# Kernel tuning notes

Measured on AMD Instinct MI355X. Metric: run time of the kernel, lower is better.

## Reference

```python
import jax, jax.numpy as jnp
import numpy as np

STRIDE = 16
A = 9
PRE_NMS_TOP_N = 6000
POST_NMS_TOP_N = 300
NMS_THRESH = 0.7
MIN_SIZE = 16
H, W = 128, 192


def _generate_anchors(base_size=16, ratios=(0.5, 1.0, 2.0), scales=(8, 16, 32)):
    base = np.array([0, 0, base_size - 1, base_size - 1], dtype=np.float64)
    w = base[2] - base[0] + 1
    h = base[3] - base[1] + 1
    x_ctr = base[0] + 0.5 * (w - 1)
    y_ctr = base[1] + 0.5 * (h - 1)
    size = w * h
    ratios = np.array(ratios)
    ws = np.round(np.sqrt(size / ratios))
    hs = np.round(ws * ratios)
    ratio_anchors = np.stack([x_ctr - 0.5 * (ws - 1), y_ctr - 0.5 * (hs - 1),
                              x_ctr + 0.5 * (ws - 1), y_ctr + 0.5 * (hs - 1)], axis=1)
    out = []
    scales = np.array(scales)
    for a in ratio_anchors:
        aw = a[2] - a[0] + 1
        ah = a[3] - a[1] + 1
        xc = a[0] + 0.5 * (aw - 1)
        yc = a[1] + 0.5 * (ah - 1)
        ws2 = aw * scales
        hs2 = ah * scales
        out.append(np.stack([xc - 0.5 * (ws2 - 1), yc - 0.5 * (hs2 - 1),
                             xc + 0.5 * (ws2 - 1), yc + 0.5 * (hs2 - 1)], axis=1))
    return np.concatenate(out, axis=0).astype(np.float32)  # [9,4]


def setup_inputs() -> dict:
    key = jax.random.key(0)
    k1, k2 = jax.random.split(key)
    scores = jax.random.uniform(k1, (1, 2 * A, H, W), dtype=jnp.float32)
    bbox_deltas = 0.1 * jax.random.normal(k2, (1, 4 * A, H, W), dtype=jnp.float32)
    im_info = jnp.array([[H * STRIDE, W * STRIDE, 1.0]], dtype=jnp.float32)
    return {"scores": scores, "bbox_deltas": bbox_deltas, "im_info": im_info}


def _proposal_forward(scores, bbox_deltas, im_info):
    anchors_base = jnp.asarray(_generate_anchors())  # [A,4]
    sc = scores[:, A:, :, :]                          # fg scores [1,A,H,W]
    h, w = sc.shape[-2], sc.shape[-1]
    shift_x = (jnp.arange(w) * STRIDE).astype(sc.dtype)
    shift_y = (jnp.arange(h) * STRIDE).astype(sc.dtype)
    sy, sx = jnp.meshgrid(shift_y, shift_x, indexing='ij')
    shifts = jnp.stack([sx.ravel(), sy.ravel(), sx.ravel(), sy.ravel()], axis=1)  # [K,4]
    anchors = (anchors_base[None, :, :] + shifts[:, None, :]).reshape(-1, 4)      # [K*A,4]

    deltas = bbox_deltas.transpose(0, 2, 3, 1).reshape(-1, 4)
    deltas = jnp.concatenate([deltas[:, :2], jnp.clip(deltas[:, 2:], -10.0, 10.0)], axis=1)
    sc = sc.transpose(0, 2, 3, 1).reshape(-1)  # [K*A]

    widths = anchors[:, 2] - anchors[:, 0] + 1.0
    heights = anchors[:, 3] - anchors[:, 1] + 1.0
    ctr_x = anchors[:, 0] + 0.5 * widths
    ctr_y = anchors[:, 1] + 0.5 * heights
    dx, dy, dw, dh = deltas[:, 0], deltas[:, 1], deltas[:, 2], deltas[:, 3]
    pcx = dx * widths + ctr_x
    pcy = dy * heights + ctr_y
    pw = jnp.exp(dw) * widths
    ph = jnp.exp(dh) * heights
    x1 = pcx - 0.5 * pw
    y1 = pcy - 0.5 * ph
    x2 = pcx + 0.5 * pw
    y2 = pcy + 0.5 * ph

    info = im_info[0]
    x1 = jnp.clip(x1, 0.0, info[1] - 1.0)
    x2 = jnp.clip(x2, 0.0, info[1] - 1.0)
    y1 = jnp.clip(y1, 0.0, info[0] - 1.0)
    y2 = jnp.clip(y2, 0.0, info[0] - 1.0)
    proposals = jnp.stack([x1, y1, x2, y2], axis=1)

    # filter_boxes: mask (instead of dropping) boxes smaller than min_size*scale
    min_sz = MIN_SIZE * info[2]
    valid = ((x2 - x1 + 1.0) >= min_sz) & ((y2 - y1 + 1.0) >= min_sz)
    masked = jnp.where(valid, sc, -jnp.inf)

    # sort desc + pre_nms_topN
    top_scores, top_idx = jax.lax.top_k(masked, PRE_NMS_TOP_N)
    boxes = proposals[top_idx]               # [PRE,4], score-descending
    tvalid = top_scores > -jnp.inf

    # pairwise IoU (torchvision convention)
    area = (boxes[:, 2] - boxes[:, 0]) * (boxes[:, 3] - boxes[:, 1])
    lt = jnp.maximum(boxes[:, None, :2], boxes[None, :, :2])
    rb = jnp.minimum(boxes[:, None, 2:], boxes[None, :, 2:])
    wh = jnp.clip(rb - lt, 0.0)
    inter = wh[..., 0] * wh[..., 1]
    iou = inter / (area[:, None] + area[None, :] - inter)  # [PRE,PRE]

    # greedy NMS over score-sorted boxes
    n = PRE_NMS_TOP_N
    def step(keep, x):
        iou_col, v, i = x
        suppressed = jnp.any(keep & (iou_col > NMS_THRESH))
        k = v & jnp.logical_not(suppressed)
        keep = keep.at[i].set(k)
        return keep, k
    keep, _ = jax.lax.scan(step, jnp.zeros((n,), dtype=bool),
                           (iou.T, tvalid, jnp.arange(n)))

    # kept boxes first (stable => score order preserved), take post_nms_topN
    order = jnp.argsort(jnp.logical_not(keep).astype(jnp.int32), stable=True)[:POST_NMS_TOP_N]
    kept = keep[order]
    out_boxes = jnp.where(kept[:, None], boxes[order], 0.0)
    output = jnp.concatenate(
        [jnp.zeros((POST_NMS_TOP_N, 1), out_boxes.dtype), out_boxes], axis=1)
    return output  # [POST,5]: (batch_idx=0, x1,y1,x2,y2); rows beyond kept count are zero


def reference(scores, bbox_deltas, im_info):
    return _proposal_forward(scores, bbox_deltas, im_info)
```

## Files before the change

kernel.cpp:

```cpp
#include <hip/hip_runtime.h>

#define N_ANCH 221184
#define HW     24576
#define Wd     192
#define AA     9
#define TOPN   6000
#define POSTN  300
#define CAND_CAP 8192
#define NWORDS 94
#define NCHUNK 47

typedef unsigned long long u64;
typedef __attribute__((ext_vector_type(2))) unsigned long long u64x2;

__device__ const float c_aw[9] = {184.f,368.f,736.f,128.f,256.f,512.f, 88.f,176.f,352.f};
__device__ const float c_ah[9] = { 96.f,192.f,384.f,128.f,256.f,512.f,176.f,352.f,704.f};

__device__ __forceinline__ float4 decode_box(int a, int cell,
                                             const float* __restrict__ deltas,
                                             float info0, float info1, float info2,
                                             bool* valid) {
    int h = cell / Wd;
    int w = cell - h * Wd;
    const float* db = deltas + (size_t)(4 * a) * HW + cell;
    float dx = db[0];
    float dy = db[HW];
    float dw = db[2 * HW];
    float dh = db[3 * HW];
    dw = fminf(fmaxf(dw, -10.f), 10.f);
    dh = fminf(fmaxf(dh, -10.f), 10.f);

    float ww = c_aw[a], hh = c_ah[a];
    float cx = 16.f * (float)w + 8.f;
    float cy = 16.f * (float)h + 8.f;

    float pcx = __fadd_rn(__fmul_rn(dx, ww), cx);
    float pcy = __fadd_rn(__fmul_rn(dy, hh), cy);
    float pw  = __fmul_rn(expf(dw), ww);
    float ph  = __fmul_rn(expf(dh), hh);
    float hpw = __fmul_rn(0.5f, pw);
    float hph = __fmul_rn(0.5f, ph);
    float x1 = __fsub_rn(pcx, hpw);
    float x2 = __fadd_rn(pcx, hpw);
    float y1 = __fsub_rn(pcy, hph);
    float y2 = __fadd_rn(pcy, hph);

    float xmax = __fsub_rn(info1, 1.f);
    float ymax = __fsub_rn(info0, 1.f);
    x1 = fminf(fmaxf(x1, 0.f), xmax);
    x2 = fminf(fmaxf(x2, 0.f), xmax);
    y1 = fminf(fmaxf(y1, 0.f), ymax);
    y2 = fminf(fmaxf(y2, 0.f), ymax);

    float msz = __fmul_rn(16.f, info2);
    *valid = (__fadd_rn(__fsub_rn(x2, x1), 1.f) >= msz) &&
             (__fadd_rn(__fsub_rn(y2, y1), 1.f) >= msz);
    return make_float4(x1, y1, x2, y2);
}

#define ZA_F4 4164
#define ZB_F4 48
__global__ __launch_bounds__(256) void init_kernel(float4* zA, float4* zB) {
    int t = blockIdx.x * 256 + threadIdx.x;
    float4 z = make_float4(0.f, 0.f, 0.f, 0.f);
    if (t < ZA_F4) zA[t] = z;
    else if (t < ZA_F4 + ZB_F4) zB[t - ZA_F4] = z;
}

__global__ __launch_bounds__(256) void decode_kernel(const float* __restrict__ scores,
                                                     const float* __restrict__ deltas,
                                                     const float* __restrict__ iminfo,
                                                     unsigned int* __restrict__ keys,
                                                     unsigned int* __restrict__ hist256) {
    __shared__ unsigned int lh[256];
    lh[threadIdx.x] = 0u;
    __syncthreads();
    int t = blockIdx.x * 256 + threadIdx.x;
    int a = t / HW;
    int cell = t - a * HW;
    float score = scores[(AA + a) * HW + cell];
    bool valid;
    (void)decode_box(a, cell, deltas, iminfo[0], iminfo[1], iminfo[2], &valid);
    unsigned int sb = __float_as_uint(score);
    unsigned int key = valid ? ((sb & 0x80000000u) ? ~sb : (sb | 0x80000000u))
                             : 0x007FFFFFu;
    keys[t] = key;
    atomicAdd(&lh[key >> 24], 1u);
    __syncthreads();
    if (lh[threadIdx.x]) atomicAdd(&hist256[threadIdx.x], lh[threadIdx.x]);
}

__global__ __launch_bounds__(1024) void midselect_kernel(const unsigned int* __restrict__ keys,
                                                         const unsigned int* __restrict__ hist256,
                                                         unsigned int* __restrict__ state) {
    __shared__ unsigned int sfx[256];
    __shared__ unsigned int h2w[16][256];
    __shared__ unsigned int sP, sRank;
    int t = threadIdx.x;
    int wv = t >> 6;
    for (int i = t; i < 16 * 256; i += 1024) ((unsigned int*)h2w)[i] = 0u;
    if (t < 256) sfx[t] = hist256[t];
    __syncthreads();
    for (int d = 1; d < 256; d <<= 1) {
        unsigned int v = 0u;
        if (t < 256 && t + d < 256) v = sfx[t + d];
        __syncthreads();
        if (t < 256) sfx[t] += v;
        __syncthreads();
    }
    if (t < 256) {
        unsigned int ge = sfx[t];
        unsigned int gt = (t < 255) ? sfx[t + 1] : 0u;
        if (ge >= TOPN && gt < TOPN) { sP = (unsigned int)t; sRank = TOPN - gt; }
    }
    __syncthreads();
    unsigned int P = sP, rank = sRank;
    const uint4* k4 = (const uint4*)keys;
    for (int i = t; i < N_ANCH / 4; i += 1024) {
        uint4 v = k4[i];
        if ((v.x >> 24) == P) atomicAdd(&h2w[wv][(v.x >> 16) & 0xFFu], 1u);
        if ((v.y >> 24) == P) atomicAdd(&h2w[wv][(v.y >> 16) & 0xFFu], 1u);
        if ((v.z >> 24) == P) atomicAdd(&h2w[wv][(v.z >> 16) & 0xFFu], 1u);
        if ((v.w >> 24) == P) atomicAdd(&h2w[wv][(v.w >> 16) & 0xFFu], 1u);
    }
    __syncthreads();
    if (t < 256) {
        unsigned int s = 0;
        #pragma unroll
        for (int wvi = 0; wvi < 16; ++wvi) s += h2w[wvi][t];
        sfx[t] = s;
    }
    __syncthreads();
    for (int d = 1; d < 256; d <<= 1) {
        unsigned int v = 0u;
        if (t < 256 && t + d < 256) v = sfx[t + d];
        __syncthreads();
        if (t < 256) sfx[t] += v;
        __syncthreads();
    }
    if (t < 256) {
        unsigned int ge = sfx[t];
        unsigned int gt = (t < 255) ? sfx[t + 1] : 0u;
        if (ge >= rank && gt < rank) {
            state[0] = (P << 24) | ((unsigned int)t << 16);
            state[2] = 0u;
        }
    }
}

__global__ __launch_bounds__(256) void compact_kernel(const unsigned int* __restrict__ keys,
                                                      unsigned int* __restrict__ state,
                                                      u64* __restrict__ cand) {
    int t = blockIdx.x * 256 + threadIdx.x;
    unsigned int k = keys[t];
    unsigned int T = state[0];
    if (k >= T) {
        unsigned int pos = atomicAdd(&state[2], 1u);
        if (pos < CAND_CAP) {
            int a = t / HW;
            int cell = t - a * HW;
            unsigned int aidx = (unsigned int)(cell * 9 + a);
            cand[pos] = ((u64)k << 32) | (u64)(~aidx);
        }
    }
}

__global__ __launch_bounds__(256) void rank_scatter_kernel(const u64* __restrict__ cand,
                                                           const float* __restrict__ deltas,
                                                           const float* __restrict__ iminfo,
                                                           float4* __restrict__ tb,
                                                           u64* __restrict__ vmask) {
    __shared__ u64 s[CAND_CAP];
    for (int j = threadIdx.x; j < CAND_CAP; j += 256) s[j] = cand[j];
    int part = threadIdx.x & 7;
    int i = blockIdx.x * 32 + (threadIdx.x >> 3);
    u64 k = cand[i];
    __syncthreads();
    const ulonglong2* sv = (const ulonglong2*)s;
    unsigned int cnt = 0;
    #pragma unroll 8
    for (int jj = part; jj < CAND_CAP / 2; jj += 8) {
        ulonglong2 v = sv[jj];
        cnt += (v.x > k) ? 1u : 0u;
        cnt += (v.y > k) ? 1u : 0u;
    }
    cnt += __shfl_xor(cnt, 1);
    cnt += __shfl_xor(cnt, 2);
    cnt += __shfl_xor(cnt, 4);
    if (part == 0 && k != 0ull && cnt < TOPN) {
        unsigned int aidx = ~((unsigned int)k);
        int a = (int)(aidx % 9u);
        int cell = (int)(aidx / 9u);
        bool valid;
        float4 box = decode_box(a, cell, deltas, iminfo[0], iminfo[1], iminfo[2], &valid);
        tb[cnt] = box;
        if ((unsigned int)(k >> 32) != 0x007FFFFFu)
            atomicOr(&vmask[cnt >> 6], 1ull << (cnt & 63));
    }
}

__global__ __launch_bounds__(64) void nms_matrix_kernel(const float4* __restrict__ tb,
                                                        u64* __restrict__ mat) {
    if (blockIdx.x < blockIdx.y) return;
    __shared__ float4 cb[64];
    int t = threadIdx.x;
    int c0 = blockIdx.x * 64;
    int col = c0 + t;
    cb[t] = (col < TOPN) ? tb[col] : make_float4(0.f, 0.f, 0.f, 0.f);
    __syncthreads();
    int row = blockIdx.y * 64 + t;
    if (row >= TOPN) return;
    float4 rb = tb[row];
    float rA = (rb.z - rb.x) * (rb.w - rb.y);
    u64 mask = 0ull;
    for (int c = 0; c < 64; ++c) {
        if (c0 + c >= TOPN) break;
        float4 b = cb[c];
        float lx = fmaxf(rb.x, b.x), ly = fmaxf(rb.y, b.y);
        float rx = fminf(rb.z, b.z), ry = fminf(rb.w, b.w);
        float iw = fmaxf(rx - lx, 0.f), ih = fmaxf(ry - ly, 0.f);
        float inter = iw * ih;
        float bA = (b.z - b.x) * (b.w - b.y);
        float iou = inter / ((rA + bA) - inter);
        if (iou > 0.7f) mask |= (1ull << c);
    }
    mat[(size_t)row * NWORDS + blockIdx.x] = mask;
}

__device__ __forceinline__ u64 rdl64(u64 v, int l) {
    unsigned int lo = (unsigned int)__builtin_amdgcn_readlane((int)(unsigned int)v, l);
    unsigned int hi = (unsigned int)__builtin_amdgcn_readlane((int)(unsigned int)(v >> 32), l);
    return ((u64)hi << 32) | (u64)lo;
}

__device__ __forceinline__ u64x2 aload_b128(const u64* p) {
    u64x2 d;
    asm volatile("global_load_dwordx4 %0, %1, off"
                 : "=v"(d) : "v"((u64)(uintptr_t)p));
    return d;
}
__device__ __forceinline__ void lgkm0() {
    asm volatile("s_waitcnt lgkmcnt(0)" ::: "memory");
}
__device__ __forceinline__ void vmwait6_fenced() {
    asm volatile("s_waitcnt vmcnt(6)" ::: "memory");
    __builtin_amdgcn_sched_barrier(0);
}

struct Dx { u64x2 a, ax, aq, b, bx, bq; };

__device__ __forceinline__ void issue_d(int c, int lane, const u64* mat, Dx& D) {
    int cc = (c < NCHUNK) ? c : (NCHUNK - 1);
    const u64* rowA = mat + (size_t)(cc * 128 + lane) * NWORDS;
    const u64* rowB = rowA + (size_t)64 * NWORDS;
    int o0 = 2 * cc;
    int o1 = (o0 + 2 <= NWORDS - 2) ? o0 + 2 : NWORDS - 2;
    int o2 = (o0 + 4 <= NWORDS - 2) ? o0 + 4 : NWORDS - 2;
    D.a  = aload_b128(rowA + o0);
    D.ax = aload_b128(rowA + o1);
    D.aq = aload_b128(rowA + o2);
    D.b  = aload_b128(rowB + o0);
    D.bx = aload_b128(rowB + o1);
    D.bq = aload_b128(rowB + o2);
}

#define DONEV 0x100000u
#define NPROP 4

__device__ __forceinline__ bool gbody(int c, int lane, const Dx& D,
                                      u64& s0, u64& s1, u64& nxp0, u64& nxp1,
                                      int& cnt, int* keptl,
                                      volatile u64* vr, volatile u64* vkm,
                                      volatile unsigned* vprog,
                                      volatile unsigned* vc0) {
    const int base = c * 128;
    u64 k0 = 0, k1 = 0, nx0 = 0, nx1 = 0, nq0 = 0, nq1 = 0;

    if ((s0 & s1) != ~0ull) {
        u64 rem0 = s0, rem1 = s1;
        while (cnt < POSTN) {
            int b;
            if (~rem0)      b = __ffsll((u64)~rem0) - 1;
            else if (~rem1) b = 64 + __ffsll((u64)~rem1) - 1;
            else break;
            if (lane == 0) keptl[cnt] = base + b;
            ++cnt;
            if (b < 64) {
                rem0 |= rdl64(D.a[0], b) | (1ull << b);
                rem1 |= rdl64(D.a[1], b);
                nx0  |= rdl64(D.ax[0], b);  nx1 |= rdl64(D.ax[1], b);
                nq0  |= rdl64(D.aq[0], b);  nq1 |= rdl64(D.aq[1], b);
                k0   |= 1ull << b;
            } else {
                int bb = b - 64;
                rem0 |= rdl64(D.b[0], bb);
                rem1 |= rdl64(D.b[1], bb) | (1ull << bb);
                nx0  |= rdl64(D.bx[0], bb); nx1 |= rdl64(D.bx[1], bb);
                nq0  |= rdl64(D.bq[0], bb); nq1 |= rdl64(D.bq[1], bb);
                k1   |= 1ull << bb;
            }
        }
        if (cnt >= POSTN) return true;
    }

    if (lane == 0) { vkm[2 * c] = k0; vkm[2 * c + 1] = k1; }
    lgkm0();
    if (lane == 0) *vc0 = (unsigned)(c + 1);

    if (c + 1 < NCHUNK) {
        int g = c - 2;
        if (g >= 0) {
            unsigned n0 = (unsigned)(g / 4) + 1u;
            unsigned n1 = (g >= 1) ? (unsigned)((g - 1) / 4) + 1u : 0u;
            unsigned n2 = (g >= 2) ? (unsigned)((g - 2) / 4) + 1u : 0u;
            unsigned n3 = (g >= 3) ? (unsigned)((g - 3) / 4) + 1u : 0u;
            for (;;) {
                unsigned p0 = vprog[0], p1 = vprog[1];
                unsigned p2 = vprog[2], p3 = vprog[3];
                if (p0 >= n0 && p1 >= n1 && p2 >= n2 && p3 >= n3) break;
                __builtin_amdgcn_s_sleep(1);
            }
        }
        const int wd = 2 * c + 2;
        u64 t0 = vr[wd]     | vr[96 + wd]     | vr[192 + wd]     | vr[288 + wd];
        u64 t1 = vr[wd + 1] | vr[96 + wd + 1] | vr[192 + wd + 1] | vr[288 + wd + 1];
        s0 = t0 | nx0 | nxp0;
        s1 = t1 | nx1 | nxp1;
        nxp0 = nq0;
        nxp1 = nq1;
    }
    return false;
}

__global__ __launch_bounds__(320, 1) void nms_scan_kernel(const u64* __restrict__ mat,
                                                          const u64* __restrict__ vmask,
                                                          const float4* __restrict__ tb,
                                                          float* __restrict__ out) {
    __shared__ int kept[POSTN];
    __shared__ u64 rfull[NPROP][96];
    __shared__ u64 keptm[NCHUNK][2];
    __shared__ unsigned prog[NPROP];
    __shared__ unsigned c0prog;
    __shared__ int cntf;

    const int tid = threadIdx.x;
    const int wid = tid >> 6;
    const int lane = tid & 63;

    volatile u64* vr = &rfull[0][0];
    volatile u64* vkm = &keptm[0][0];
    volatile unsigned* vprog = prog;
    volatile unsigned* vc0 = &c0prog;

    u64 pr0 = 0ull, pr1 = 0ull;
    Dx DA, DB;
    if (wid == 0) {
        issue_d(0, lane, mat, DA);
    } else {
        const int w = wid - 1;
        if (w == 0) {
            pr0 = ~vmask[lane];
            pr1 = (lane < NWORDS - 64) ? ~vmask[64 + lane] : 0ull;
        }
        vr[w * 96 + lane] = pr0;
        if (lane < 32) vr[w * 96 + 64 + lane] = (lane < NWORDS - 64) ? pr1 : 0ull;
    }
    if (tid < NPROP) vprog[tid] = 0u;
    if (tid == 0) { *vc0 = 0u; cntf = 0; }
    __syncthreads();

    if (wid == 0) {
        int cnt = 0;
        u64 s0 = vr[0], s1 = vr[1];
        u64 nxp0 = 0ull, nxp1 = 0ull;
        bool done = false;
        for (int p = 0; p < (NCHUNK + 1) / 2 && !done; ++p) {
            int c0 = 2 * p;
            issue_d(c0 + 1, lane, mat, DB);
            vmwait6_fenced();
            done = gbody(c0, lane, DA, s0, s1, nxp0, nxp1, cnt, kept,
                         vr, vkm, vprog, vc0);
            if (done || c0 + 1 >= NCHUNK) break;
            issue_d(c0 + 2, lane, mat, DA);
            vmwait6_fenced();
            done = gbody(c0 + 1, lane, DB, s0, s1, nxp0, nxp1, cnt, kept,
                         vr, vkm, vprog, vc0);
        }
        asm volatile("s_waitcnt vmcnt(0)" ::: "memory");
        if (lane == 0) cntf = cnt;
        lgkm0();
        if (lane == 0) *vc0 = DONEV;
    } else {
        const int w = wid - 1;
        const u64 lmask = (lane < NWORDS - 64) ? ~0ull : 0ull;
        const int l1w = (lane < NWORDS - 64) ? (64 + lane) : (NWORDS - 1);
        u64 r0 = pr0, r1 = pr1;
        for (int j = w; j < NCHUNK; j += NPROP) {
            bool dead = false;
            for (;;) {
                unsigned v = *vc0;
                if (v >= DONEV) { dead = true; break; }
                if (v > (unsigned)j) break;
                __builtin_amdgcn_s_sleep(1);
            }
            if (dead) break;
            u64 k0 = vkm[2 * j], k1 = vkm[2 * j + 1];
            const int base = j * 128;
            while (k0 | k1) {
                int idxs[8];
                #pragma unroll
                for (int q = 0; q < 8; ++q) {
                    int b = -1;
                    if (k0)      { b = __ffsll(k0) - 1;      k0 &= k0 - 1; }
                    else if (k1) { b = 64 + __ffsll(k1) - 1; k1 &= k1 - 1; }
                    idxs[q] = b;
                }
                u64 v0[8], v1[8];
                #pragma unroll
                for (int q = 0; q < 8; ++q) {
                    v0[q] = 0ull; v1[q] = 0ull;
                    if (idxs[q] >= 0) {
                        const u64* row = mat + (size_t)(base + idxs[q]) * NWORDS;
                        v0[q] = row[lane];
                        v1[q] = row[l1w];
                    }
                }
                #pragma unroll
                for (int q = 0; q < 8; ++q) { r0 |= v0[q]; r1 |= v1[q] & lmask; }
            }
            vr[w * 96 + lane] = r0;
            if (lane < NWORDS - 64) vr[w * 96 + 64 + lane] = r1;
            lgkm0();
            if (lane == 0) vprog[w] = (unsigned)((j - w) / NPROP) + 1u;
        }
    }

    __syncthreads();
    const int cn = cntf;
    for (int r = tid; r < POSTN; r += 320) {
        float4 b = make_float4(0.f, 0.f, 0.f, 0.f);
        if (r < cn) b = tb[kept[r]];
        float* o = out + r * 5;
        o[0] = 0.f; o[1] = b.x; o[2] = b.y; o[3] = b.z; o[4] = b.w;
    }
}

extern "C" void kernel_launch(void* const* d_in, const int* in_sizes, int n_in,
                              void* d_out, int out_size, void* d_ws, size_t ws_size,
                              hipStream_t stream) {
    const float* scores = (const float*)d_in[0];
    const float* deltas = (const float*)d_in[1];
    const float* iminfo = (const float*)d_in[2];
    float* out = (float*)d_out;

    char* ws = (char*)d_ws;
    unsigned int* keys    = (unsigned int*)(ws + 0);
    unsigned int* hist256 = (unsigned int*)(ws + 884736);
    unsigned int* state   = (unsigned int*)(ws + 885760);
    u64*          cand    = (u64*)(ws + 885824);
    float4*       tb      = (float4*)(ws + 951360);
    u64*          vmask   = (u64*)(ws + 1047616);
    u64*          mat     = (u64*)(ws + 1048384);

    const int NB = N_ANCH / 256;

    init_kernel<<<17, 256, 0, stream>>>((float4*)hist256, (float4*)vmask);
    decode_kernel<<<NB, 256, 0, stream>>>(scores, deltas, iminfo, keys, hist256);
    midselect_kernel<<<1, 1024, 0, stream>>>(keys, hist256, state);
    compact_kernel<<<NB, 256, 0, stream>>>(keys, state, cand);
    rank_scatter_kernel<<<CAND_CAP / 32, 256, 0, stream>>>(cand, deltas, iminfo, tb, vmask);
    nms_matrix_kernel<<<dim3(NWORDS, NWORDS), 64, 0, stream>>>(tb, mat);
    nms_scan_kernel<<<1, 320, 0, stream>>>(mat, vmask, tb, out);
}
```

Before: 268.6 us.

## Extend NMS scan lookahead by one chunk, prefetch deeper, raise scan wave priority

The serial scan wave now loads a fourth 128-bit mask word pair per row, so suppression for chunk c+3 is built locally. The helper waves therefore only need to have finished chunk c-3 before the scan continues, which gives them one more chunk of slack. Loads are issued one chunk earlier (the second buffer is primed before the loop and refilled after each body), and the scan wave runs at raised priority. The s_sleep calls in the spin-wait loops are removed to cut wake-up latency. The cost is more VGPRs and readlanes per kept box, plus busier spinning that may compete with the helper waves for issue slots.

```diff
diff --git a/kernel.cpp b/kernel.cpp
--- a/kernel.cpp
+++ b/kernel.cpp
@@ -242,12 +242,12 @@
 __device__ __forceinline__ void lgkm0() {
     asm volatile("s_waitcnt lgkmcnt(0)" ::: "memory");
 }
-__device__ __forceinline__ void vmwait6_fenced() {
-    asm volatile("s_waitcnt vmcnt(6)" ::: "memory");
+__device__ __forceinline__ void vmwait8_fenced() {
+    asm volatile("s_waitcnt vmcnt(8)" ::: "memory");
     __builtin_amdgcn_sched_barrier(0);
 }
 
-struct Dx { u64x2 a, ax, aq, b, bx, bq; };
+struct Dx { u64x2 a, ax, aq, ar, b, bx, bq, br; };
 
 __device__ __forceinline__ void issue_d(int c, int lane, const u64* mat, Dx& D) {
     int cc = (c < NCHUNK) ? c : (NCHUNK - 1);
@@ -256,25 +256,31 @@
     int o0 = 2 * cc;
     int o1 = (o0 + 2 <= NWORDS - 2) ? o0 + 2 : NWORDS - 2;
     int o2 = (o0 + 4 <= NWORDS - 2) ? o0 + 4 : NWORDS - 2;
+    int o3 = (o0 + 6 <= NWORDS - 2) ? o0 + 6 : NWORDS - 2;
     D.a  = aload_b128(rowA + o0);
     D.ax = aload_b128(rowA + o1);
     D.aq = aload_b128(rowA + o2);
+    D.ar = aload_b128(rowA + o3);
     D.b  = aload_b128(rowB + o0);
     D.bx = aload_b128(rowB + o1);
     D.bq = aload_b128(rowB + o2);
+    D.br = aload_b128(rowB + o3);
 }
 
 #define DONEV 0x100000u
 #define NPROP 4
 
 __device__ __forceinline__ bool gbody(int c, int lane, const Dx& D,
-                                      u64& s0, u64& s1, u64& nxp0, u64& nxp1,
+                                      u64& s0, u64& s1,
+                                      u64& nqP0, u64& nqP1,
+                                      u64& nrP0, u64& nrP1,
+                                      u64& nrPP0, u64& nrPP1,
                                       int& cnt, int* keptl,
                                       volatile u64* vr, volatile u64* vkm,
                                       volatile unsigned* vprog,
                                       volatile unsigned* vc0) {
     const int base = c * 128;
-    u64 k0 = 0, k1 = 0, nx0 = 0, nx1 = 0, nq0 = 0, nq1 = 0;
+    u64 k0 = 0, k1 = 0, nx0 = 0, nx1 = 0, nq0 = 0, nq1 = 0, nr0 = 0, nr1 = 0;
 
     if ((s0 & s1) != ~0ull) {
         u64 rem0 = s0, rem1 = s1;
@@ -290,6 +296,7 @@
                 rem1 |= rdl64(D.a[1], b);
                 nx0  |= rdl64(D.ax[0], b);  nx1 |= rdl64(D.ax[1], b);
                 nq0  |= rdl64(D.aq[0], b);  nq1 |= rdl64(D.aq[1], b);
+                nr0  |= rdl64(D.ar[0], b);  nr1 |= rdl64(D.ar[1], b);
                 k0   |= 1ull << b;
             } else {
                 int bb = b - 64;
@@ -297,6 +304,7 @@
                 rem1 |= rdl64(D.b[1], bb) | (1ull << bb);
                 nx0  |= rdl64(D.bx[0], bb); nx1 |= rdl64(D.bx[1], bb);
                 nq0  |= rdl64(D.bq[0], bb); nq1 |= rdl64(D.bq[1], bb);
+                nr0  |= rdl64(D.br[0], bb); nr1 |= rdl64(D.br[1], bb);
                 k1   |= 1ull << bb;
             }
         }
@@ -308,7 +316,7 @@
     if (lane == 0) *vc0 = (unsigned)(c + 1);
 
     if (c + 1 < NCHUNK) {
-        int g = c - 2;
+        int g = c - 3;
         if (g >= 0) {
             unsigned n0 = (unsigned)(g / 4) + 1u;
             unsigned n1 = (g >= 1) ? (unsigned)((g - 1) / 4) + 1u : 0u;
@@ -318,17 +326,17 @@
                 unsigned p0 = vprog[0], p1 = vprog[1];
                 unsigned p2 = vprog[2], p3 = vprog[3];
                 if (p0 >= n0 && p1 >= n1 && p2 >= n2 && p3 >= n3) break;
-                __builtin_amdgcn_s_sleep(1);
             }
         }
         const int wd = 2 * c + 2;
         u64 t0 = vr[wd]     | vr[96 + wd]     | vr[192 + wd]     | vr[288 + wd];
         u64 t1 = vr[wd + 1] | vr[96 + wd + 1] | vr[192 + wd + 1] | vr[288 + wd + 1];
-        s0 = t0 | nx0 | nxp0;
-        s1 = t1 | nx1 | nxp1;
-        nxp0 = nq0;
-        nxp1 = nq1;
-    }
+        s0 = t0 | nx0 | nqP0 | nrPP0;
+        s1 = t1 | nx1 | nqP1 | nrPP1;
+    }
+    nrPP0 = nrP0; nrPP1 = nrP1;
+    nrP0  = nr0;  nrP1  = nr1;
+    nqP0  = nq0;  nqP1  = nq1;
     return false;
 }
 
@@ -356,6 +364,7 @@
     Dx DA, DB;
     if (wid == 0) {
         issue_d(0, lane, mat, DA);
+        issue_d(1, lane, mat, DB);
     } else {
         const int w = wid - 1;
         if (w == 0) {
@@ -370,23 +379,26 @@
     __syncthreads();
 
     if (wid == 0) {
+        __builtin_amdgcn_s_setprio(1);
         int cnt = 0;
         u64 s0 = vr[0], s1 = vr[1];
-        u64 nxp0 = 0ull, nxp1 = 0ull;
+        u64 nqP0 = 0, nqP1 = 0, nrP0 = 0, nrP1 = 0, nrPP0 = 0, nrPP1 = 0;
         bool done = false;
         for (int p = 0; p < (NCHUNK + 1) / 2 && !done; ++p) {
             int c0 = 2 * p;
-            issue_d(c0 + 1, lane, mat, DB);
-            vmwait6_fenced();
-            done = gbody(c0, lane, DA, s0, s1, nxp0, nxp1, cnt, kept,
-                         vr, vkm, vprog, vc0);
+            vmwait8_fenced();
+            done = gbody(c0, lane, DA, s0, s1, nqP0, nqP1, nrP0, nrP1,
+                         nrPP0, nrPP1, cnt, kept, vr, vkm, vprog, vc0);
             if (done || c0 + 1 >= NCHUNK) break;
             issue_d(c0 + 2, lane, mat, DA);
-            vmwait6_fenced();
-            done = gbody(c0 + 1, lane, DB, s0, s1, nxp0, nxp1, cnt, kept,
-                         vr, vkm, vprog, vc0);
+            vmwait8_fenced();
+            done = gbody(c0 + 1, lane, DB, s0, s1, nqP0, nqP1, nrP0, nrP1,
+                         nrPP0, nrPP1, cnt, kept, vr, vkm, vprog, vc0);
+            if (done) break;
+            issue_d(c0 + 3, lane, mat, DB);
         }
         asm volatile("s_waitcnt vmcnt(0)" ::: "memory");
+        __builtin_amdgcn_s_setprio(0);
         if (lane == 0) cntf = cnt;
         lgkm0();
         if (lane == 0) *vc0 = DONEV;
@@ -401,7 +413,6 @@
                 unsigned v = *vc0;
                 if (v >= DONEV) { dead = true; break; }
                 if (v > (unsigned)j) break;
-                __builtin_amdgcn_s_sleep(1);
             }
             if (dead) break;
             u64 k0 = vkm[2 * j], k1 = vkm[2 * j + 1];
```

New measurement: 275.2 us. 1.02x slower.
